# Optimization experiments

Hardware: AMD Instinct MI355X
Metric: run time of the kernel (lower is better)

## Reference

```python
import jax, jax.numpy as jnp
import numpy as np

D_MODEL = 1024
NUM_HEADS = 16
HEAD_DIM = D_MODEL // NUM_HEADS  # 64
# NOTE: the original module passes scale=attention_head_size, so scores are
# MULTIPLIED by head_dim (64), not divided by sqrt(head_dim). Faithful quirk.
SCALE = float(HEAD_DIM)


def setup_inputs() -> dict:
    key = jax.random.key(0)
    ks = jax.random.split(key, 6)
    bs, s, d = 2, 2048, D_MODEL
    q = jax.random.normal(ks[0], (bs, s, d), dtype=jnp.float32)
    k = jax.random.normal(ks[1], (bs, s, d), dtype=jnp.float32)
    v = jax.random.normal(ks[2], (bs, s, d), dtype=jnp.float32)
    # nn.Linear weights, shape (out, in); no bias (qkv_bias=False)
    init = 1.0 / np.sqrt(d)
    Wq = jax.random.uniform(ks[3], (d, d), jnp.float32, -init, init)
    Wk = jax.random.uniform(ks[4], (d, d), jnp.float32, -init, init)
    Wv = jax.random.uniform(ks[5], (d, d), jnp.float32, -init, init)
    return {"q": q, "k": k, "v": v, "Wq": Wq, "Wk": Wk, "Wv": Wv}


def _split_heads(x):
    bs, s, _ = x.shape
    return x.reshape(bs, s, NUM_HEADS, HEAD_DIM).transpose(0, 2, 1, 3)  # bhsd


def reference(q, k, v, Wq, Wk, Wv):
    bs, s, d = q.shape
    qh = _split_heads(q @ Wq.T)  # [b,h,s,hd]
    kh = _split_heads(k @ Wk.T)
    vh = _split_heads(v @ Wv.T)
    sims = jnp.einsum('bhqd,bhkd->bhqk', qh, kh) * SCALE
    attn = jax.nn.softmax(sims, axis=-1)
    out = jnp.einsum('bhqk,bhkd->bhqd', attn, vh)  # [b,h,s,hd]
    out = out.transpose(0, 2, 1, 3).reshape(bs, s, d)
    return out
```

## Files before the change

### kernel.cpp

```cpp
#include <hip/hip_runtime.h>


typedef _Float16 half4 __attribute__((ext_vector_type(4)));
typedef _Float16 half8 __attribute__((ext_vector_type(8)));
typedef float floatx4 __attribute__((ext_vector_type(4)));

#define MFMA_F16(a, b, c) __builtin_amdgcn_mfma_f32_16x16x32_f16((a), (b), (c), 0, 0, 0)

constexpr int SEQ = 2048;
constexpr int DM = 1024;
constexpr int NH = 16;
constexpr int HD = 64;
constexpr float QSCALE = 92.33248261689366f;

__device__ __forceinline__ void gl2lds16(const _Float16* g, _Float16* l) {
  __builtin_amdgcn_global_load_lds(
      (const __attribute__((address_space(1))) void*)g,
      (__attribute__((address_space(3))) void*)l, 16, 0, 0);
}

__device__ inline void split4(const float4 f, half4& h, half4& l) {
  h[0] = (_Float16)f.x; l[0] = (_Float16)(f.x - (float)h[0]);
  h[1] = (_Float16)f.y; l[1] = (_Float16)(f.y - (float)h[1]);
  h[2] = (_Float16)f.z; l[2] = (_Float16)(f.z - (float)h[2]);
  h[3] = (_Float16)f.w; l[3] = (_Float16)(f.w - (float)h[3]);
}

__global__ __launch_bounds__(256) void convert_kernel(
    const float* __restrict__ x, const float* __restrict__ W,
    _Float16* __restrict__ xh, _Float16* __restrict__ xl,
    _Float16* __restrict__ Wh, _Float16* __restrict__ Wl, int do_lo)
{
  if (blockIdx.x < 4096) {
    int idx = blockIdx.x * 256 + threadIdx.x;
    float4 f = ((const float4*)x)[idx];
    half4 h, l; split4(f, h, l);
    *(half4*)(xh + (size_t)idx * 4) = h;
    if (do_lo) *(half4*)(xl + (size_t)idx * 4) = l;
  } else {
    int idx = (blockIdx.x - 4096) * 256 + threadIdx.x;
    float4 f = ((const float4*)W)[idx];
    half4 h, l; split4(f, h, l);
    *(half4*)(Wh + (size_t)idx * 4) = h;
    if (do_lo) *(half4*)(Wl + (size_t)idx * 4) = l;
  }
}

__global__ __launch_bounds__(256, 1) void proj_kernel(
    const _Float16* __restrict__ Ahg, const _Float16* __restrict__ Alg,
    const _Float16* __restrict__ Bhg, const _Float16* __restrict__ Blg,
    _Float16* __restrict__ yh, _Float16* __restrict__ yl,
    float scale, int three)
{
  __shared__ __align__(16) _Float16 Ahs[128][64];
  __shared__ __align__(16) _Float16 Als[128][64];
  __shared__ __align__(16) _Float16 Bhs[128][64];
  __shared__ __align__(16) _Float16 Bls[128][64];

  const int tid = threadIdx.x;
  const int bm = blockIdx.x;
  const int bn = blockIdx.y;
  const int lane = tid & 63, l15 = lane & 15, quad = lane >> 4;
  const int w = tid >> 6, wm = w >> 1, wn = w & 1;

  const int r8 = lane >> 3;
  const int cp8 = (((lane & 7) ^ r8)) * 8;
  int grow[4]; _Float16* la[4]; _Float16* lal[4]; _Float16* lb[4]; _Float16* lbl[4];
  #pragma unroll
  for (int i = 0; i < 4; i++) {
    const int g = w * 4 + i;
    grow[i] = g * 8 + r8;
    la[i]  = &Ahs[0][0] + g * 512;
    lal[i] = &Als[0][0] + g * 512;
    lb[i]  = &Bhs[0][0] + g * 512;
    lbl[i] = &Bls[0][0] + g * 512;
  }

  floatx4 acc[4][4];
  #pragma unroll
  for (int mt = 0; mt < 4; mt++)
    #pragma unroll
    for (int nt = 0; nt < 4; nt++)
      acc[mt][nt] = (floatx4){0.f, 0.f, 0.f, 0.f};

  for (int kk = 0; kk < DM; kk += 64) {
    __syncthreads();
    #pragma unroll
    for (int i = 0; i < 4; i++) {
      const size_t ga = (size_t)(bm * 128 + grow[i]) * DM + kk + cp8;
      const size_t gb = (size_t)(bn * 128 + grow[i]) * DM + kk + cp8;
      gl2lds16(Ahg + ga, la[i]);
      gl2lds16(Bhg + gb, lb[i]);
      if (three) {
        gl2lds16(Alg + ga, lal[i]);
        gl2lds16(Blg + gb, lbl[i]);
      }
    }
    __syncthreads();

    #pragma unroll
    for (int kc = 0; kc < 2; kc++) {
      const int swz = ((kc * 4 + quad) ^ (l15 & 7)) * 8;
      half8 ah[4], bh_[4], al[4], bl[4];
      #pragma unroll
      for (int t = 0; t < 4; t++) {
        ah[t]  = *(const half8*)&Ahs[wm * 64 + t * 16 + l15][swz];
        bh_[t] = *(const half8*)&Bhs[wn * 64 + t * 16 + l15][swz];
        if (three) {
          al[t] = *(const half8*)&Als[wm * 64 + t * 16 + l15][swz];
          bl[t] = *(const half8*)&Bls[wn * 64 + t * 16 + l15][swz];
        }
      }
      if (three) {
        #pragma unroll
        for (int mt = 0; mt < 4; mt++)
          #pragma unroll
          for (int nt = 0; nt < 4; nt++) {
            floatx4 t0 = MFMA_F16(ah[mt], bh_[nt], acc[mt][nt]);
            t0 = MFMA_F16(ah[mt], bl[nt], t0);
            acc[mt][nt] = MFMA_F16(al[mt], bh_[nt], t0);
          }
      } else {
        #pragma unroll
        for (int mt = 0; mt < 4; mt++)
          #pragma unroll
          for (int nt = 0; nt < 4; nt++)
            acc[mt][nt] = MFMA_F16(ah[mt], bh_[nt], acc[mt][nt]);
      }
    }
  }

  #pragma unroll
  for (int mt = 0; mt < 4; mt++)
    #pragma unroll
    for (int nt = 0; nt < 4; nt++)
      #pragma unroll
      for (int r = 0; r < 4; r++) {
        int gm = bm * 128 + wm * 64 + mt * 16 + quad * 4 + r;
        int gn = bn * 128 + wn * 64 + nt * 16 + l15;
        int b = gm >> 11, s = gm & 2047;
        int h = gn >> 6, d = gn & 63;
        size_t idx = ((size_t)(b * NH + h) * SEQ + s) * HD + d;
        float val = acc[mt][nt][r] * scale;
        _Float16 hi = (_Float16)val;
        yh[idx] = hi;
        if (three) yl[idx] = (_Float16)(val - (float)hi);
      }
}

__global__ __launch_bounds__(256) void transpose_v(const _Float16* __restrict__ vh,
                                                   _Float16* __restrict__ vhT)
{
  __shared__ __align__(16) _Float16 T[128][72];
  const int bh = blockIdx.x, sc = blockIdx.y, tid = threadIdx.x;
  const _Float16* src = vh + ((size_t)bh * SEQ + sc * 128) * HD;
  #pragma unroll
  for (int i = 0; i < 4; i++) {
    int c = i * 256 + tid, row = c >> 3, off = (c & 7) * 8;
    *(half8*)&T[row][off] = *(const half8*)(src + (size_t)row * HD + off);
  }
  __syncthreads();
  _Float16* dst = vhT + (size_t)bh * HD * SEQ + sc * 128;
  #pragma unroll
  for (int i = 0; i < 4; i++) {
    int c = i * 256 + tid, hd = c >> 4, off = (c & 15) * 8;
    int base32 = off & ~31, qsel = (off >> 3) & 3;
    half8 vv;
    #pragma unroll
    for (int j = 0; j < 8; j++) {
      int s_local = base32 + 16 * (j >> 2) + 4 * qsel + (j & 3);
      vv[j] = T[s_local][hd];
    }
    *(half8*)(dst + (size_t)hd * SEQ + off) = vv;
  }
}

__global__ __launch_bounds__(256, 4) void flash_kernel(
    const _Float16* __restrict__ qh_hi, const _Float16* __restrict__ qh_lo,
    const _Float16* __restrict__ kh_hi, const _Float16* __restrict__ kh_lo,
    const _Float16* __restrict__ vhT, float* __restrict__ Op, float2* __restrict__ ml)
{
  __shared__ __align__(16) _Float16 Kh[64][64];
  __shared__ __align__(16) _Float16 Kl[64][64];
  __shared__ __align__(16) _Float16 Vt[64][64];

  const int id = blockIdx.x;
  const int seq_ = id >> 3;
  const int bh = (id & 7) + 8 * (seq_ & 3);
  const int rem = seq_ >> 2;
  const int qb = rem & 15;
  const int kh = rem >> 4;
  const int tid = threadIdx.x;
  const int wq = tid >> 6;
  const int lane = tid & 63, l15 = lane & 15, quad = lane >> 4;

  const size_t bh_off = (size_t)bh * SEQ * HD;
  const _Float16* __restrict__ kh_p = kh_hi + bh_off;
  const _Float16* __restrict__ kl_p = kh_lo + bh_off;
  const _Float16* __restrict__ vt_p = vhT + (size_t)bh * HD * SEQ;
  const int qrow0 = qb * 128 + wq * 32;

  half8 bqh[2][2], bql[2][2];
  #pragma unroll
  for (int g = 0; g < 2; g++) {
    const _Float16* qp_h = qh_hi + bh_off + (size_t)(qrow0 + g * 16 + l15) * HD;
    const _Float16* qp_l = qh_lo + bh_off + (size_t)(qrow0 + g * 16 + l15) * HD;
    #pragma unroll
    for (int kc = 0; kc < 2; kc++) {
      bqh[g][kc] = *(const half8*)(qp_h + kc * 32 + quad * 8);
      bql[g][kc] = *(const half8*)(qp_l + kc * 32 + quad * 8);
    }
  }

  const int r8 = lane >> 3;
  const int cp8 = ((lane & 7) ^ r8) * 8;

  float m_[2] = {-3.0e38f, -3.0e38f};
  float l_[2] = {0.f, 0.f};
  floatx4 Oacc[2][4];
  #pragma unroll
  for (int g = 0; g < 2; g++)
    #pragma unroll
    for (int nd = 0; nd < 4; nd++) Oacc[g][nd] = (floatx4){0.f, 0.f, 0.f, 0.f};

  const int kt0 = kh * 16;
  for (int kt = kt0; kt < kt0 + 16; kt++) {
    const int kbase = kt * 64;
    __syncthreads();
    #pragma unroll
    for (int i = 0; i < 2; i++) {
      const int g = wq * 2 + i;
      const int r = g * 8 + r8;
      gl2lds16(kh_p + (size_t)(kbase + r) * HD + cp8, &Kh[0][0] + g * 512);
      gl2lds16(kl_p + (size_t)(kbase + r) * HD + cp8, &Kl[0][0] + g * 512);
      gl2lds16(vt_p + (size_t)r * SEQ + kbase + cp8, &Vt[0][0] + g * 512);
    }
    __syncthreads();

    floatx4 sacc[2][4];
    #pragma unroll
    for (int nt = 0; nt < 4; nt++) {
      const int r7 = l15 & 7;
      half8 akh0 = *(const half8*)&Kh[nt * 16 + l15][((0 * 4 + quad) ^ r7) * 8];
      half8 akh1 = *(const half8*)&Kh[nt * 16 + l15][((1 * 4 + quad) ^ r7) * 8];
      half8 akl0 = *(const half8*)&Kl[nt * 16 + l15][((0 * 4 + quad) ^ r7) * 8];
      half8 akl1 = *(const half8*)&Kl[nt * 16 + l15][((1 * 4 + quad) ^ r7) * 8];
      #pragma unroll
      for (int g = 0; g < 2; g++) {
        floatx4 s4 = (floatx4){0.f, 0.f, 0.f, 0.f};
        s4 = MFMA_F16(akh0, bqh[g][0], s4);
        s4 = MFMA_F16(akh1, bqh[g][1], s4);
        s4 = MFMA_F16(akh0, bql[g][0], s4);
        s4 = MFMA_F16(akh1, bql[g][1], s4);
        s4 = MFMA_F16(akl0, bqh[g][0], s4);
        s4 = MFMA_F16(akl1, bqh[g][1], s4);
        sacc[g][nt] = s4;
      }
    }

    half8 av[4][2];
    {
      const int r7 = l15 & 7;
      #pragma unroll
      for (int nd = 0; nd < 4; nd++) {
        av[nd][0] = *(const half8*)&Vt[nd * 16 + l15][((0 * 4 + quad) ^ r7) * 8];
        av[nd][1] = *(const half8*)&Vt[nd * 16 + l15][((1 * 4 + quad) ^ r7) * 8];
      }
    }

    #pragma unroll
    for (int g = 0; g < 2; g++) {
      float rmax = sacc[g][0][0];
      #pragma unroll
      for (int nt = 0; nt < 4; nt++)
        #pragma unroll
        for (int r = 0; r < 4; r++) rmax = fmaxf(rmax, sacc[g][nt][r]);
      rmax = fmaxf(rmax, __shfl_xor(rmax, 16, 64));
      rmax = fmaxf(rmax, __shfl_xor(rmax, 32, 64));
      const float mnew = fmaxf(m_[g], rmax);
      const float alpha = exp2f(m_[g] - mnew);
      m_[g] = mnew;

      float rsum = 0.f;
      #pragma unroll
      for (int nt = 0; nt < 4; nt++)
        #pragma unroll
        for (int r = 0; r < 4; r++) {
          float p = exp2f(sacc[g][nt][r] - mnew);
          sacc[g][nt][r] = p;
          rsum += p;
        }
      rsum += __shfl_xor(rsum, 16, 64);
      rsum += __shfl_xor(rsum, 32, 64);
      l_[g] = l_[g] * alpha + rsum;

      half8 bp8[2];
      #pragma unroll
      for (int kc = 0; kc < 2; kc++)
        #pragma unroll
        for (int j = 0; j < 8; j++)
          bp8[kc][j] = (_Float16)sacc[g][2 * kc + (j >> 2)][j & 3];

      #pragma unroll
      for (int nd = 0; nd < 4; nd++) {
        Oacc[g][nd][0] *= alpha; Oacc[g][nd][1] *= alpha;
        Oacc[g][nd][2] *= alpha; Oacc[g][nd][3] *= alpha;
        Oacc[g][nd] = MFMA_F16(av[nd][0], bp8[0], Oacc[g][nd]);
        Oacc[g][nd] = MFMA_F16(av[nd][1], bp8[1], Oacc[g][nd]);
      }
    }
  }

  const size_t fqbase = (size_t)bh * SEQ + qrow0;
  #pragma unroll
  for (int g = 0; g < 2; g++) {
    const size_t fq = fqbase + g * 16 + l15;
    float* ob = Op + ((size_t)kh * 65536 + fq) * HD;
    #pragma unroll
    for (int nd = 0; nd < 4; nd++) {
      float4 vv;
      vv.x = Oacc[g][nd][0]; vv.y = Oacc[g][nd][1];
      vv.z = Oacc[g][nd][2]; vv.w = Oacc[g][nd][3];
      *(float4*)(ob + nd * 16 + quad * 4) = vv;
    }
    if (quad == 0) ml[kh * 65536 + fq] = make_float2(m_[g], l_[g]);
  }
}

__global__ __launch_bounds__(256) void merge_kernel(const float* __restrict__ Op,
                                                    const float2* __restrict__ ml,
                                                    float* __restrict__ out)
{
  const int tid = threadIdx.x;
  const int fq = blockIdx.x * 64 + (tid >> 2);
  const int dp = (tid & 3) * 16;
  float2 m0 = ml[fq], m1 = ml[65536 + fq];
  float M = fmaxf(m0.x, m1.x);
  float w0 = exp2f(m0.x - M), w1 = exp2f(m1.x - M);
  float rinv = 1.0f / (m0.y * w0 + m1.y * w1);
  int bh = fq >> 11, s = fq & 2047, b = bh >> 4, h = bh & 15;
  float* ob = out + ((size_t)(b * SEQ + s)) * DM + h * HD + dp;
  const float* p0 = Op + (size_t)fq * HD + dp;
  const float* p1 = p0 + (size_t)65536 * HD;
  #pragma unroll
  for (int j = 0; j < 4; j++) {
    float4 a = *(const float4*)(p0 + 4 * j);
    float4 c = *(const float4*)(p1 + 4 * j);
    float4 r;
    r.x = (a.x * w0 + c.x * w1) * rinv;
    r.y = (a.y * w0 + c.y * w1) * rinv;
    r.z = (a.z * w0 + c.z * w1) * rinv;
    r.w = (a.w * w0 + c.w * w1) * rinv;
    *(float4*)(ob + 4 * j) = r;
  }
}

extern "C" void kernel_launch(void* const* d_in, const int* in_sizes, int n_in,
                              void* d_out, int out_size, void* d_ws, size_t ws_size,
                              hipStream_t stream) {
  const float* q  = (const float*)d_in[0];
  const float* k  = (const float*)d_in[1];
  const float* v  = (const float*)d_in[2];
  const float* Wq = (const float*)d_in[3];
  const float* Wk = (const float*)d_in[4];
  const float* Wv = (const float*)d_in[5];
  float* out = (float*)d_out;

  char* W = (char*)d_ws;
  const size_t MiB = 1ull << 20;
  _Float16* qh_hi = (_Float16*)(W + 0 * MiB);
  _Float16* qh_lo = (_Float16*)(W + 8 * MiB);
  _Float16* kh_hi = (_Float16*)(W + 16 * MiB);
  _Float16* kh_lo = (_Float16*)(W + 24 * MiB);
  _Float16* vhT   = (_Float16*)(W + 32 * MiB);
  _Float16* vh    = (_Float16*)(W + 40 * MiB);
  _Float16* xh    = (_Float16*)(W + 48 * MiB);
  _Float16* xl    = (_Float16*)(W + 56 * MiB);
  _Float16* Wh    = (_Float16*)(W + 64 * MiB);
  _Float16* Wl    = (_Float16*)(W + 66 * MiB);
  float*    Op    = (float*)  (W + 40 * MiB);
  float2*   mlp   = (float2*) (W + 72 * MiB);

  convert_kernel<<<5120, 256, 0, stream>>>(q, Wq, xh, xl, Wh, Wl, 1);
  proj_kernel<<<dim3(32, 8), 256, 0, stream>>>(xh, xl, Wh, Wl, qh_hi, qh_lo, QSCALE, 1);
  convert_kernel<<<5120, 256, 0, stream>>>(k, Wk, xh, xl, Wh, Wl, 1);
  proj_kernel<<<dim3(32, 8), 256, 0, stream>>>(xh, xl, Wh, Wl, kh_hi, kh_lo, 1.0f, 1);
  convert_kernel<<<5120, 256, 0, stream>>>(v, Wv, xh, xl, Wh, Wl, 0);
  proj_kernel<<<dim3(32, 8), 256, 0, stream>>>(xh, xl, Wh, Wl, vh, vh, 1.0f, 0);

  transpose_v<<<dim3(32, 16), 256, 0, stream>>>(vh, vhT);
  flash_kernel<<<1024, 256, 0, stream>>>(qh_hi, qh_lo, kh_hi, kh_lo, vhT, Op, mlp);
  merge_kernel<<<1024, 256, 0, stream>>>(Op, mlp, out);
}
```

Measured before the change: 321.8 us.

## Fuse activation conversion into projection GEMM, batch Q/K, split flash keys three ways

Activation fp32-to-fp16 hi/lo splitting now happens inside the projection kernel. Each block loads fp32 tiles into LDS and splits them on the fly, so the separate convert passes over q/k/v are gone, and only the weights are pre-converted in a single launch. Q and K projections run in one launch via blockIdx.z, the M tile is halved to 64 for more blocks, and occupancy hints change. Flash attention splits the keys into three chunks with fp16 partial outputs, and the merge combines three partials. The fp16 partial outputs lose some precision in exchange for less memory traffic.

```diff
diff --git a/kernel.cpp b/kernel.cpp
--- a/kernel.cpp
+++ b/kernel.cpp
@@ -13,7 +13,7 @@
 constexpr int HD = 64;
 constexpr float QSCALE = 92.33248261689366f;
 
-__device__ __forceinline__ void gl2lds16(const _Float16* g, _Float16* l) {
+__device__ __forceinline__ void gl2lds16(const void* g, void* l) {
   __builtin_amdgcn_global_load_lds(
       (const __attribute__((address_space(1))) void*)g,
       (__attribute__((address_space(3))) void*)l, 16, 0, 0);
@@ -26,36 +26,36 @@
   h[3] = (_Float16)f.w; l[3] = (_Float16)(f.w - (float)h[3]);
 }
 
-__global__ __launch_bounds__(256) void convert_kernel(
-    const float* __restrict__ x, const float* __restrict__ W,
-    _Float16* __restrict__ xh, _Float16* __restrict__ xl,
-    _Float16* __restrict__ Wh, _Float16* __restrict__ Wl, int do_lo)
+__global__ __launch_bounds__(256) void convert_w(
+    const float* __restrict__ Wq, const float* __restrict__ Wk,
+    const float* __restrict__ Wv, _Float16* __restrict__ Wbase)
 {
-  if (blockIdx.x < 4096) {
-    int idx = blockIdx.x * 256 + threadIdx.x;
-    float4 f = ((const float4*)x)[idx];
-    half4 h, l; split4(f, h, l);
-    *(half4*)(xh + (size_t)idx * 4) = h;
-    if (do_lo) *(half4*)(xl + (size_t)idx * 4) = l;
-  } else {
-    int idx = (blockIdx.x - 4096) * 256 + threadIdx.x;
-    float4 f = ((const float4*)W)[idx];
-    half4 h, l; split4(f, h, l);
-    *(half4*)(Wh + (size_t)idx * 4) = h;
-    if (do_lo) *(half4*)(Wl + (size_t)idx * 4) = l;
-  }
-}
-
-__global__ __launch_bounds__(256, 1) void proj_kernel(
-    const _Float16* __restrict__ Ahg, const _Float16* __restrict__ Alg,
-    const _Float16* __restrict__ Bhg, const _Float16* __restrict__ Blg,
-    _Float16* __restrict__ yh, _Float16* __restrict__ yl,
-    float scale, int three)
+  const int z = blockIdx.x >> 10;
+  const int idx = (blockIdx.x & 1023) * 256 + threadIdx.x;
+  const float* __restrict__ src = (z == 0) ? Wq : (z == 1) ? Wk : Wv;
+  float4 f = ((const float4*)src)[idx];
+  half4 h, l; split4(f, h, l);
+  _Float16* Wh = Wbase + (size_t)z * 2097152;
+  *(half4*)(Wh + (size_t)idx * 4) = h;
+  if (z < 2) *(half4*)(Wh + 1048576 + (size_t)idx * 4) = l;
+}
+
+template<int THREE>
+__global__ __launch_bounds__(256, 3) void proj_kernel(
+    const float* __restrict__ x0, const float* __restrict__ x1,
+    const _Float16* __restrict__ Wb,
+    _Float16* __restrict__ yh0, _Float16* __restrict__ yl0,
+    _Float16* __restrict__ yh1, _Float16* __restrict__ yl1,
+    float sc0, float sc1)
 {
-  __shared__ __align__(16) _Float16 Ahs[128][64];
-  __shared__ __align__(16) _Float16 Als[128][64];
+  __shared__ __align__(16) float    Af[64][64];
   __shared__ __align__(16) _Float16 Bhs[128][64];
-  __shared__ __align__(16) _Float16 Bls[128][64];
+  __shared__ __align__(16) _Float16 Bls[THREE ? 128 : 1][64];
+
+  const int z = blockIdx.z;
+  const float* __restrict__ x = z ? x1 : x0;
+  const _Float16* __restrict__ Whg = Wb + (size_t)z * 2097152;
+  const _Float16* __restrict__ Wlg = Whg + 1048576;
 
   const int tid = threadIdx.x;
   const int bm = blockIdx.x;
@@ -63,22 +63,12 @@
   const int lane = tid & 63, l15 = lane & 15, quad = lane >> 4;
   const int w = tid >> 6, wm = w >> 1, wn = w & 1;
 
-  const int r8 = lane >> 3;
-  const int cp8 = (((lane & 7) ^ r8)) * 8;
-  int grow[4]; _Float16* la[4]; _Float16* lal[4]; _Float16* lb[4]; _Float16* lbl[4];
-  #pragma unroll
-  for (int i = 0; i < 4; i++) {
-    const int g = w * 4 + i;
-    grow[i] = g * 8 + r8;
-    la[i]  = &Ahs[0][0] + g * 512;
-    lal[i] = &Als[0][0] + g * 512;
-    lb[i]  = &Bhs[0][0] + g * 512;
-    lbl[i] = &Bls[0][0] + g * 512;
-  }
-
-  floatx4 acc[4][4];
-  #pragma unroll
-  for (int mt = 0; mt < 4; mt++)
+  const int r4 = lane >> 4, pc16 = lane & 15;
+  const int r8 = lane >> 3, pc8 = lane & 7;
+
+  floatx4 acc[2][4];
+  #pragma unroll
+  for (int mt = 0; mt < 2; mt++)
     #pragma unroll
     for (int nt = 0; nt < 4; nt++)
       acc[mt][nt] = (floatx4){0.f, 0.f, 0.f, 0.f};
@@ -87,56 +77,75 @@
     __syncthreads();
     #pragma unroll
     for (int i = 0; i < 4; i++) {
-      const size_t ga = (size_t)(bm * 128 + grow[i]) * DM + kk + cp8;
-      const size_t gb = (size_t)(bn * 128 + grow[i]) * DM + kk + cp8;
-      gl2lds16(Ahg + ga, la[i]);
-      gl2lds16(Bhg + gb, lb[i]);
-      if (three) {
-        gl2lds16(Alg + ga, lal[i]);
-        gl2lds16(Blg + gb, lbl[i]);
+      const int g = w * 4 + i;
+      {
+        const int row = g * 4 + r4;
+        const int lc = pc16 ^ (row & 15);
+        gl2lds16(x + (size_t)(bm * 64 + row) * DM + kk + lc * 4,
+                 &Af[0][0] + g * 256);
+      }
+      {
+        const int row = g * 8 + r8;
+        const int lc = pc8 ^ (r8 & 7);
+        gl2lds16(Whg + (size_t)(bn * 128 + row) * DM + kk + lc * 8,
+                 &Bhs[0][0] + g * 512);
+        if (THREE)
+          gl2lds16(Wlg + (size_t)(bn * 128 + row) * DM + kk + lc * 8,
+                   &Bls[0][0] + g * 512);
       }
     }
     __syncthreads();
 
     #pragma unroll
     for (int kc = 0; kc < 2; kc++) {
-      const int swz = ((kc * 4 + quad) ^ (l15 & 7)) * 8;
-      half8 ah[4], bh_[4], al[4], bl[4];
-      #pragma unroll
-      for (int t = 0; t < 4; t++) {
-        ah[t]  = *(const half8*)&Ahs[wm * 64 + t * 16 + l15][swz];
-        bh_[t] = *(const half8*)&Bhs[wn * 64 + t * 16 + l15][swz];
-        if (three) {
-          al[t] = *(const half8*)&Als[wm * 64 + t * 16 + l15][swz];
-          bl[t] = *(const half8*)&Bls[wn * 64 + t * 16 + l15][swz];
+      half8 ah[2], al[2];
+      #pragma unroll
+      for (int mt = 0; mt < 2; mt++) {
+        const float* rp = &Af[wm * 32 + mt * 16 + l15][0];
+        float4 f0 = *(const float4*)(rp + ((kc * 8 + quad * 2) ^ l15) * 4);
+        float4 f1 = *(const float4*)(rp + ((kc * 8 + quad * 2 + 1) ^ l15) * 4);
+        half4 h0, l0, h1, l1;
+        split4(f0, h0, l0);
+        split4(f1, h1, l1);
+        #pragma unroll
+        for (int j = 0; j < 4; j++) {
+          ah[mt][j] = h0[j]; ah[mt][j + 4] = h1[j];
+          al[mt][j] = l0[j]; al[mt][j + 4] = l1[j];
         }
       }
-      if (three) {
+      half8 bh_[4], bl[4];
+      #pragma unroll
+      for (int nt = 0; nt < 4; nt++) {
+        const int row = wn * 64 + nt * 16 + l15;
+        const int swz = ((kc * 4 + quad) ^ (l15 & 7)) * 8;
+        bh_[nt] = *(const half8*)&Bhs[row][swz];
+        if (THREE) bl[nt] = *(const half8*)&Bls[row][swz];
+      }
+      #pragma unroll
+      for (int mt = 0; mt < 2; mt++)
         #pragma unroll
-        for (int mt = 0; mt < 4; mt++)
-          #pragma unroll
-          for (int nt = 0; nt < 4; nt++) {
+        for (int nt = 0; nt < 4; nt++) {
+          if (THREE) {
             floatx4 t0 = MFMA_F16(ah[mt], bh_[nt], acc[mt][nt]);
             t0 = MFMA_F16(ah[mt], bl[nt], t0);
             acc[mt][nt] = MFMA_F16(al[mt], bh_[nt], t0);
+          } else {
+            acc[mt][nt] = MFMA_F16(ah[mt], bh_[nt], acc[mt][nt]);
           }
-      } else {
-        #pragma unroll
-        for (int mt = 0; mt < 4; mt++)
-          #pragma unroll
-          for (int nt = 0; nt < 4; nt++)
-            acc[mt][nt] = MFMA_F16(ah[mt], bh_[nt], acc[mt][nt]);
-      }
-    }
-  }
-
-  #pragma unroll
-  for (int mt = 0; mt < 4; mt++)
+        }
+    }
+  }
+
+  const float scale = z ? sc1 : sc0;
+  _Float16* yh = z ? yh1 : yh0;
+  _Float16* yl = z ? yl1 : yl0;
+  #pragma unroll
+  for (int mt = 0; mt < 2; mt++)
     #pragma unroll
     for (int nt = 0; nt < 4; nt++)
       #pragma unroll
       for (int r = 0; r < 4; r++) {
-        int gm = bm * 128 + wm * 64 + mt * 16 + quad * 4 + r;
+        int gm = bm * 64 + wm * 32 + mt * 16 + quad * 4 + r;
         int gn = bn * 128 + wn * 64 + nt * 16 + l15;
         int b = gm >> 11, s = gm & 2047;
         int h = gn >> 6, d = gn & 63;
@@ -144,7 +153,7 @@
         float val = acc[mt][nt][r] * scale;
         _Float16 hi = (_Float16)val;
         yh[idx] = hi;
-        if (three) yl[idx] = (_Float16)(val - (float)hi);
+        if (THREE) yl[idx] = (_Float16)(val - (float)hi);
       }
 }
 
@@ -175,10 +184,11 @@
   }
 }
 
-__global__ __launch_bounds__(256, 4) void flash_kernel(
+__global__ __launch_bounds__(256, 6) void flash_kernel(
     const _Float16* __restrict__ qh_hi, const _Float16* __restrict__ qh_lo,
     const _Float16* __restrict__ kh_hi, const _Float16* __restrict__ kh_lo,
-    const _Float16* __restrict__ vhT, float* __restrict__ Op, float2* __restrict__ ml)
+    const _Float16* __restrict__ vhT, _Float16* __restrict__ Op,
+    float2* __restrict__ ml)
 {
   __shared__ __align__(16) _Float16 Kh[64][64];
   __shared__ __align__(16) _Float16 Kl[64][64];
@@ -189,7 +199,7 @@
   const int bh = (id & 7) + 8 * (seq_ & 3);
   const int rem = seq_ >> 2;
   const int qb = rem & 15;
-  const int kh = rem >> 4;
+  const int split = rem >> 4;
   const int tid = threadIdx.x;
   const int wq = tid >> 6;
   const int lane = tid & 63, l15 = lane & 15, quad = lane >> 4;
@@ -223,8 +233,9 @@
     #pragma unroll
     for (int nd = 0; nd < 4; nd++) Oacc[g][nd] = (floatx4){0.f, 0.f, 0.f, 0.f};
 
-  const int kt0 = kh * 16;
-  for (int kt = kt0; kt < kt0 + 16; kt++) {
+  const int kt_begin = split * 11;
+  const int kt_end = (split == 2) ? 32 : (kt_begin + 11);
+  for (int kt = kt_begin; kt < kt_end; kt++) {
     const int kbase = kt * 64;
     __syncthreads();
     #pragma unroll
@@ -315,42 +326,46 @@
   #pragma unroll
   for (int g = 0; g < 2; g++) {
     const size_t fq = fqbase + g * 16 + l15;
-    float* ob = Op + ((size_t)kh * 65536 + fq) * HD;
+    _Float16* ob = Op + ((size_t)split * 65536 + fq) * HD;
     #pragma unroll
     for (int nd = 0; nd < 4; nd++) {
-      float4 vv;
-      vv.x = Oacc[g][nd][0]; vv.y = Oacc[g][nd][1];
-      vv.z = Oacc[g][nd][2]; vv.w = Oacc[g][nd][3];
-      *(float4*)(ob + nd * 16 + quad * 4) = vv;
-    }
-    if (quad == 0) ml[kh * 65536 + fq] = make_float2(m_[g], l_[g]);
-  }
-}
-
-__global__ __launch_bounds__(256) void merge_kernel(const float* __restrict__ Op,
+      half4 hv;
+      hv[0] = (_Float16)Oacc[g][nd][0];
+      hv[1] = (_Float16)Oacc[g][nd][1];
+      hv[2] = (_Float16)Oacc[g][nd][2];
+      hv[3] = (_Float16)Oacc[g][nd][3];
+      *(half4*)(ob + nd * 16 + quad * 4) = hv;
+    }
+    if (quad == 0) ml[(size_t)split * 65536 + fq] = make_float2(m_[g], l_[g]);
+  }
+}
+
+__global__ __launch_bounds__(256) void merge_kernel(const _Float16* __restrict__ Op,
                                                     const float2* __restrict__ ml,
                                                     float* __restrict__ out)
 {
   const int tid = threadIdx.x;
   const int fq = blockIdx.x * 64 + (tid >> 2);
   const int dp = (tid & 3) * 16;
-  float2 m0 = ml[fq], m1 = ml[65536 + fq];
-  float M = fmaxf(m0.x, m1.x);
-  float w0 = exp2f(m0.x - M), w1 = exp2f(m1.x - M);
-  float rinv = 1.0f / (m0.y * w0 + m1.y * w1);
+  float2 ma = ml[fq], mb = ml[65536 + fq], mc = ml[131072 + fq];
+  float M = fmaxf(ma.x, fmaxf(mb.x, mc.x));
+  float wa = exp2f(ma.x - M), wb = exp2f(mb.x - M), wc = exp2f(mc.x - M);
+  float rinv = 1.0f / (ma.y * wa + mb.y * wb + mc.y * wc);
   int bh = fq >> 11, s = fq & 2047, b = bh >> 4, h = bh & 15;
   float* ob = out + ((size_t)(b * SEQ + s)) * DM + h * HD + dp;
-  const float* p0 = Op + (size_t)fq * HD + dp;
-  const float* p1 = p0 + (size_t)65536 * HD;
+  const _Float16* pa = Op + (size_t)fq * HD + dp;
+  const _Float16* pb = pa + (size_t)65536 * HD;
+  const _Float16* pc = pb + (size_t)65536 * HD;
   #pragma unroll
   for (int j = 0; j < 4; j++) {
-    float4 a = *(const float4*)(p0 + 4 * j);
-    float4 c = *(const float4*)(p1 + 4 * j);
+    half4 a = *(const half4*)(pa + 4 * j);
+    half4 c = *(const half4*)(pb + 4 * j);
+    half4 d = *(const half4*)(pc + 4 * j);
     float4 r;
-    r.x = (a.x * w0 + c.x * w1) * rinv;
-    r.y = (a.y * w0 + c.y * w1) * rinv;
-    r.z = (a.z * w0 + c.z * w1) * rinv;
-    r.w = (a.w * w0 + c.w * w1) * rinv;
+    r.x = ((float)a[0] * wa + (float)c[0] * wb + (float)d[0] * wc) * rinv;
+    r.y = ((float)a[1] * wa + (float)c[1] * wb + (float)d[1] * wc) * rinv;
+    r.z = ((float)a[2] * wa + (float)c[2] * wb + (float)d[2] * wc) * rinv;
+    r.w = ((float)a[3] * wa + (float)c[3] * wb + (float)d[3] * wc) * rinv;
     *(float4*)(ob + 4 * j) = r;
   }
 }
@@ -374,21 +389,16 @@
   _Float16* kh_lo = (_Float16*)(W + 24 * MiB);
   _Float16* vhT   = (_Float16*)(W + 32 * MiB);
   _Float16* vh    = (_Float16*)(W + 40 * MiB);
-  _Float16* xh    = (_Float16*)(W + 48 * MiB);
-  _Float16* xl    = (_Float16*)(W + 56 * MiB);
-  _Float16* Wh    = (_Float16*)(W + 64 * MiB);
-  _Float16* Wl    = (_Float16*)(W + 66 * MiB);
-  float*    Op    = (float*)  (W + 40 * MiB);
-  float2*   mlp   = (float2*) (W + 72 * MiB);
-
-  convert_kernel<<<5120, 256, 0, stream>>>(q, Wq, xh, xl, Wh, Wl, 1);
-  proj_kernel<<<dim3(32, 8), 256, 0, stream>>>(xh, xl, Wh, Wl, qh_hi, qh_lo, QSCALE, 1);
-  convert_kernel<<<5120, 256, 0, stream>>>(k, Wk, xh, xl, Wh, Wl, 1);
-  proj_kernel<<<dim3(32, 8), 256, 0, stream>>>(xh, xl, Wh, Wl, kh_hi, kh_lo, 1.0f, 1);
-  convert_kernel<<<5120, 256, 0, stream>>>(v, Wv, xh, xl, Wh, Wl, 0);
-  proj_kernel<<<dim3(32, 8), 256, 0, stream>>>(xh, xl, Wh, Wl, vh, vh, 1.0f, 0);
-
+  _Float16* Wbase = (_Float16*)(W + 48 * MiB);
+  _Float16* Oph   = (_Float16*)(W + 40 * MiB);
+  float2*   mlp   = (float2*)  (W + 64 * MiB);
+
+  convert_w<<<3072, 256, 0, stream>>>(Wq, Wk, Wv, Wbase);
+  proj_kernel<1><<<dim3(64, 8, 2), 256, 0, stream>>>(
+      q, k, Wbase, qh_hi, qh_lo, kh_hi, kh_lo, QSCALE, 1.0f);
+  proj_kernel<0><<<dim3(64, 8, 1), 256, 0, stream>>>(
+      v, v, Wbase + (size_t)2 * 2097152, vh, vh, vh, vh, 1.0f, 1.0f);
   transpose_v<<<dim3(32, 16), 256, 0, stream>>>(vh, vhT);
-  flash_kernel<<<1024, 256, 0, stream>>>(qh_hi, qh_lo, kh_hi, kh_lo, vhT, Op, mlp);
-  merge_kernel<<<1024, 256, 0, stream>>>(Op, mlp, out);
-}
+  flash_kernel<<<1536, 256, 0, stream>>>(qh_hi, qh_lo, kh_hi, kh_lo, vhT, Oph, mlp);
+  merge_kernel<<<1024, 256, 0, stream>>>(Oph, mlp, out);
+}
```

New measurement: 700.6 us. +117.7%, slower.
